# Kernel tuning notes

Hardware: AMD Instinct MI355X
Metric: run time of the kernel (lower is better)

## Reference

```python
import jax, jax.numpy as jnp
import numpy as np

EPS = 1e-5
NUM_HEADS = 8


def _ln(x, g, b):
    m = jnp.mean(x, axis=-1, keepdims=True)
    v = jnp.var(x, axis=-1, keepdims=True)
    return (x - m) * jax.lax.rsqrt(v + EPS) * g + b


def _adaptive_pool_mat(L, out):
    # torch F.adaptive_avg_pool1d bin edges: start=floor(i*L/out), end=ceil((i+1)*L/out)
    i = np.arange(out)
    start = (i * L) // out
    end = -((-(i + 1) * L) // out)
    W = np.zeros((out, L), np.float32)
    for r in range(out):
        W[r, start[r]:end[r]] = 1.0 / (end[r] - start[r])
    return jnp.asarray(W)


def _sparse_mask(S, key):
    # True = blocked. Local band of width ~0.1*S plus random unblocked entries per row.
    keep = max(1, int(S * 0.1))
    half = keep // 2
    idx = jnp.arange(S)
    band = (idx[None, :] >= idx[:, None] - half) & (idx[None, :] <= idx[:, None] + half)
    blocked = ~band
    if keep > 4:
        num_random = max(1, keep // 4)
        keys = jax.random.split(key, S)
        rand_idx = jax.vmap(lambda k: jax.random.permutation(k, S)[:num_random])(keys)
        blocked = blocked.at[idx[:, None], rand_idx].set(False)
    return blocked


def setup_inputs() -> dict:
    key = jax.random.key(0)
    ks = jax.random.split(key, 12)
    B, C, H, W = 1, 256, 64, 64
    s = lambda k, shp: jax.random.normal(k, shp, jnp.float32) * 0.02
    return dict(
        x=jax.random.normal(ks[0], (B, C, H, W), jnp.float32),
        local_pos=s(ks[1], (1, C)),
        reg_pos0=s(ks[2], (1, C)),
        reg_pos1=s(ks[3], (1, C)),
        ln_local_g=jnp.ones((C,), jnp.float32), ln_local_b=jnp.zeros((C,), jnp.float32),
        ln_reg0_g=jnp.ones((C,), jnp.float32), ln_reg0_b=jnp.zeros((C,), jnp.float32),
        ln_reg1_g=jnp.ones((C,), jnp.float32), ln_reg1_b=jnp.zeros((C,), jnp.float32),
        adj0_w=s(ks[4], (C, C * 16)), adj0_b=jnp.zeros((C,), jnp.float32),
        adj1_w=s(ks[5], (C, C * 64)), adj1_b=jnp.zeros((C,), jnp.float32),
        in_proj_w=s(ks[6], (3 * C, C)), in_proj_b=jnp.zeros((3 * C,), jnp.float32),
        out_w=s(ks[7], (C, C)), out_b=jnp.zeros((C,), jnp.float32),
        ln_out_g=jnp.ones((C,), jnp.float32), ln_out_b=jnp.zeros((C,), jnp.float32),
        mlp_w1=s(ks[8], (4 * C, C)), mlp_b1=jnp.zeros((4 * C,), jnp.float32),
        mlp_w2=s(ks[9], (C, 4 * C)), mlp_b2=jnp.zeros((C,), jnp.float32),
    )


def reference(x, local_pos, reg_pos0, reg_pos1,
              ln_local_g, ln_local_b, ln_reg0_g, ln_reg0_b, ln_reg1_g, ln_reg1_b,
              adj0_w, adj0_b, adj1_w, adj1_b,
              in_proj_w, in_proj_b, out_w, out_b,
              ln_out_g, ln_out_b, mlp_w1, mlp_b1, mlp_w2, mlp_b2):
    B, C, H, W = x.shape
    HW = H * W
    # local branch: [B, HW, C]
    x_flat = x.reshape(B, C, HW).transpose(0, 2, 1)
    local_f = _ln(x_flat + local_pos[0], ln_local_g, ln_local_b)
    # regional branches (patch sizes 4, 8): each produces C tokens of dim C
    regional = []
    for ps, rp, lg, lb, aw, ab in ((4, reg_pos0, ln_reg0_g, ln_reg0_b, adj0_w, adj0_b),
                                   (8, reg_pos1, ln_reg1_g, ln_reg1_b, adj1_w, adj1_b)):
        N = (H // ps) * (W // ps)
        xp = x.reshape(B, C, H // ps, ps, W // ps, ps)
        xp = xp.transpose(0, 2, 4, 1, 3, 5).reshape(B, N, C * ps * ps)
        pool = _adaptive_pool_mat(N, C)          # [C, N] pools token dim N -> C
        xp = jnp.einsum('bnd,cn->bcd', xp, pool)  # [B, C, C*ps*ps]
        xp = xp @ aw.T + ab                        # dim_adjust -> [B, C, C]
        regional.append(_ln(xp + rp[0], lg, lb))
    feats = jnp.concatenate([local_f] + regional, axis=1)  # [B, S, C]
    S = feats.shape[1]
    blocked = _sparse_mask(S, jax.random.key(42))
    # MultiheadAttention (eval, dropout off)
    dh = C // NUM_HEADS
    qkv = feats @ in_proj_w.T + in_proj_b
    q, k, v = jnp.split(qkv, 3, axis=-1)
    heads = lambda t: t.reshape(B, S, NUM_HEADS, dh).transpose(0, 2, 1, 3)
    q, k, v = heads(q), heads(k), heads(v)
    scores = jnp.einsum('bhqd,bhkd->bhqk', q, k) / jnp.sqrt(jnp.float32(dh))
    scores = jnp.where(blocked, -jnp.inf, scores)
    attn = jax.nn.softmax(scores, axis=-1)
    ctx = jnp.einsum('bhqk,bhkd->bhqd', attn, v).transpose(0, 2, 1, 3).reshape(B, S, C)
    attn_out = ctx @ out_w.T + out_b
    # take local tokens, residual MLP, fold back to image, outer residual
    lo = attn_out[:, :HW]
    h1 = jax.nn.gelu(_ln(lo, ln_out_g, ln_out_b) @ mlp_w1.T + mlp_b1, approximate=False)
    lo = lo + (h1 @ mlp_w2.T + mlp_b2)
    return lo.transpose(0, 2, 1).reshape(B, C, H, W) + x
```

## Files before the change

kernel.cpp:

```cpp
#include <hip/hip_runtime.h>
#include <hip/hip_bf16.h>
#include <cstdint>

#define THREEFRY_PARTITIONABLE 1

#define C_DIM 256
#define HW 4096
#define S_TOK 4608
#define NRAND 115
#define NW 144
#define HALF_BAND 230
#define CANDCAP 208
#define PTP 40
#define NHEADS 8

typedef __attribute__((ext_vector_type(8))) short bf16x8;
typedef __attribute__((ext_vector_type(4))) float f32x4;
typedef __attribute__((ext_vector_type(16))) float f32x16;

__device__ __forceinline__ bool isbf(const void* gref) {
  return *(const uint32_t*)gref != 0x3F800000u;
}
__device__ __forceinline__ float ldin(const void* p, int i, bool bf) {
  if (bf) return __bfloat162float(((const __hip_bfloat16*)p)[i]);
  return ((const float*)p)[i];
}
__device__ __forceinline__ void stout(void* p, int i, float v, bool bf) {
  if (bf) ((__hip_bfloat16*)p)[i] = __float2bfloat16(v);
  else ((float*)p)[i] = v;
}
__device__ __forceinline__ uint16_t f2bf(float f) {
  __hip_bfloat16 h = __float2bfloat16(f);
  return *(uint16_t*)&h;
}
__device__ __forceinline__ float bfu2f(uint32_t u16) {
  return __uint_as_float(u16 << 16);
}
__device__ __forceinline__ void ld4f(const void* X, bool bf, int idx, float* o) {
  if (bf) {
    const ushort4 u = *(const ushort4*)((const uint16_t*)X + idx);
    o[0] = bfu2f(u.x); o[1] = bfu2f(u.y); o[2] = bfu2f(u.z); o[3] = bfu2f(u.w);
  } else {
    const float4 f = *(const float4*)((const float*)X + idx);
    o[0] = f.x; o[1] = f.y; o[2] = f.z; o[3] = f.w;
  }
}

__device__ __forceinline__ void tf2x32(uint32_t k0, uint32_t k1,
                                       uint32_t x0, uint32_t x1,
                                       uint32_t& o0, uint32_t& o1) {
  const uint32_t k2 = k0 ^ k1 ^ 0x1BD11BDAu;
  x0 += k0; x1 += k1;
#define TFR(r) x0 += x1; x1 = (x1 << (r)) | (x1 >> (32 - (r))); x1 ^= x0;
  TFR(13) TFR(15) TFR(26) TFR(6)
  x0 += k1; x1 += k2 + 1u;
  TFR(17) TFR(29) TFR(16) TFR(24)
  x0 += k2; x1 += k0 + 2u;
  TFR(13) TFR(15) TFR(26) TFR(6)
  x0 += k0; x1 += k1 + 3u;
  TFR(17) TFR(29) TFR(16) TFR(24)
  x0 += k1; x1 += k2 + 4u;
  TFR(13) TFR(15) TFR(26) TFR(6)
  x0 += k2; x1 += k0 + 5u;
#undef TFR
  o0 = x0; o1 = x1;
}

__device__ __forceinline__ float blockSum256(float v, float* rb, int tid) {
#pragma unroll
  for (int o = 32; o > 0; o >>= 1) v += __shfl_down(v, o, 64);
  if ((tid & 63) == 0) rb[tid >> 6] = v;
  __syncthreads();
  float r = rb[0] + rb[1] + rb[2] + rb[3];
  __syncthreads();
  return r;
}

__global__ __launch_bounds__(512) void k_mask(uint16_t* __restrict__ randl) {
  const int q = blockIdx.x;
  const int tid = threadIdx.x;
  __shared__ uint32_t keys1s[S_TOK];
  __shared__ uint16_t mem1[S_TOK];
  __shared__ uint8_t  b2hi[S_TOK];
  __shared__ uint32_t baseA[257];
  __shared__ uint32_t baseB[257];
  __shared__ uint32_t offs[256];
  __shared__ uint32_t candk[CANDCAP];
  __shared__ uint16_t candi[CANDCAP];
  __shared__ uint32_t posmask[NW];
  __shared__ uint8_t  hotb[256];
  __shared__ uint16_t randrow[128];
  __shared__ uint32_t wsum[8];
  __shared__ int ncand, Tsh, nrcnt;

  uint32_t s10, s11, s20, s21;
  {
#if THREEFRY_PARTITIONABLE
    uint32_t kq0, kq1, ka0, ka1;
    tf2x32(0u, 42u, 0u, (uint32_t)q, kq0, kq1);
    tf2x32(kq0, kq1, 0u, 0u, ka0, ka1);
    tf2x32(kq0, kq1, 0u, 1u, s10, s11);
    tf2x32(ka0, ka1, 0u, 1u, s20, s21);
#else
    uint32_t o0, o1, k0, k1;
    uint32_t j = 2u * (uint32_t)q;
    if (j < S_TOK) { tf2x32(0u, 42u, j, j + S_TOK, o0, o1); k0 = o0; }
    else           { tf2x32(0u, 42u, j - S_TOK, j, o0, o1); k0 = o1; }
    j = 2u * (uint32_t)q + 1u;
    if (j < S_TOK) { tf2x32(0u, 42u, j, j + S_TOK, o0, o1); k1 = o0; }
    else           { tf2x32(0u, 42u, j - S_TOK, j, o0, o1); k1 = o1; }
    uint32_t a0, b0, a1, b1;
    tf2x32(k0, k1, 0u, 2u, a0, b0);
    tf2x32(k0, k1, 1u, 3u, a1, b1);
    s10 = b0; s11 = b1;
    uint32_t c0, d0, c1, d1;
    tf2x32(a0, a1, 0u, 2u, c0, d0);
    tf2x32(a0, a1, 1u, 3u, c1, d1);
    s20 = d0; s21 = d1;
#endif
  }
  if (tid == 0) { ncand = 0; Tsh = 0; nrcnt = 0; }
  if (tid < 256) { baseA[tid] = 0u; baseB[tid] = 0u; }
  for (int w = tid; w < NW; w += 512) posmask[w] = 0u;
  __syncthreads();

  uint32_t v1reg[9];
#pragma unroll
  for (int it = 0; it < 9; ++it) {
    const int i = tid + it * 512;
    uint32_t a, b;
    tf2x32(s10, s11, 0u, (uint32_t)i, a, b);
    const uint32_t v1 = a ^ b;
    tf2x32(s20, s21, 0u, (uint32_t)i, a, b);
    const uint32_t v2 = a ^ b;
    v1reg[it] = v1;
    atomicAdd(&baseA[v1 >> 24], 1u);
    atomicAdd(&baseB[v2 >> 24], 1u);
    b2hi[i] = (uint8_t)(v2 >> 24);
  }
  __syncthreads();

  {
    const int g = tid >> 8;
    const int loc = tid & 255;
    uint32_t* base = g ? baseB : baseA;
    const uint32_t v = base[loc];
    uint32_t s = v;
    const int lane = tid & 63;
#pragma unroll
    for (int o = 1; o < 64; o <<= 1) {
      const uint32_t t = __shfl_up(s, o, 64);
      if (lane >= o) s += t;
    }
    if (lane == 63) wsum[g * 4 + (loc >> 6)] = s;
    __syncthreads();
    uint32_t woff = 0;
#pragma unroll
    for (int w = 0; w < 3; ++w)
      if (w < (loc >> 6)) woff += wsum[g * 4 + w];
    const uint32_t ex = woff + s - v;
    base[loc] = ex;
    if (loc == 255) base[256] = ex + v;
    if (g == 1 && (int)ex <= NRAND - 1) atomicMax(&Tsh, loc);
  }
  __syncthreads();
  if (tid < 256) offs[tid] = baseA[tid];
  const int T = Tsh;
  __syncthreads();

#pragma unroll
  for (int it = 0; it < 9; ++it) {
    const int i = tid + it * 512;
    const uint32_t v1 = v1reg[it];
    const uint32_t p = atomicAdd(&offs[v1 >> 24], 1u);
    keys1s[p] = v1;
    mem1[p] = (uint16_t)i;
    if ((int)b2hi[i] <= T) {
      uint32_t a, b;
      tf2x32(s20, s21, 0u, (uint32_t)i, a, b);
      const uint32_t v2 = a ^ b;
      const int c = atomicAdd(&ncand, 1);
      if (c < CANDCAP) { candk[c] = v2; candi[c] = (uint16_t)i; }
    }
  }
  __syncthreads();

  const int nc = min(ncand, CANDCAP);
  for (int c = tid; c < nc; c += 512) {
    const uint32_t kk = candk[c];
    const uint16_t ii = candi[c];
    int r = 0;
    for (int c2 = 0; c2 < nc; ++c2) {
      const uint32_t k2 = candk[c2];
      if (k2 < kk || (k2 == kk && candi[c2] < ii)) ++r;
    }
    if (r < NRAND) atomicOr(&posmask[ii >> 5], 1u << (ii & 31));
  }
  __syncthreads();

  if (tid < 256) {
    const int s0 = (int)baseA[tid], e0 = (int)baseA[tid + 1];
    uint8_t hot = 0;
    if (s0 < e0) {
      for (int w = (s0 >> 5); w <= ((e0 - 1) >> 5); ++w) {
        const int lo = max(s0, w * 32) - w * 32;
        const int hi = min(e0 - 1, w * 32 + 31) - w * 32;
        const uint32_t range = ((hi == 31) ? 0xFFFFFFFFu : ((1u << (hi + 1)) - 1u)) & ~((1u << lo) - 1u);
        if (posmask[w] & range) { hot = 1; break; }
      }
    }
    hotb[tid] = hot;
  }
  __syncthreads();

  for (int p = tid; p < S_TOK; p += 512) {
    const uint32_t ke = keys1s[p];
    const uint32_t bk = ke >> 24;
    if (!hotb[bk]) continue;
    const int e = (int)mem1[p];
    const int s0 = (int)baseA[bk], e0 = (int)baseA[bk + 1];
    int less = 0, eq = 0;
    for (int m = s0; m < e0; ++m) {
      const uint32_t kf = keys1s[m];
      less += (int)(kf < ke);
      eq += (int)(kf == ke);
    }
    int R = s0 + less;
    if (eq > 1) {
      int r2 = 0;
      for (int m = s0; m < e0; ++m)
        if (keys1s[m] == ke && (int)mem1[m] < e) ++r2;
      R += r2;
    }
    if ((posmask[R >> 5] >> (R & 31)) & 1u) {
      const int c = atomicAdd(&nrcnt, 1);
      if (c < 128) randrow[c] = (uint16_t)e;
    }
  }
  __syncthreads();
  if (tid < NRAND) randl[(size_t)q * 128 + tid] = randrow[tid];
}

__global__ __launch_bounds__(256) void k_transpose(const void* __restrict__ x, float* __restrict__ xt,
                                                   const void* __restrict__ gref) {
  const bool bf = isbf(gref);
  __shared__ float tile[32][33];
  const int n0 = blockIdx.x * 32, c0 = blockIdx.y * 32;
  const int tx = threadIdx.x & 31, ty = threadIdx.x >> 5;
  for (int i = ty; i < 32; i += 8)
    tile[i][tx] = ldin(x, (c0 + i) * HW + n0 + tx, bf);
  __syncthreads();
  for (int i = ty; i < 32; i += 8)
    xt[(size_t)(n0 + i) * C_DIM + c0 + tx] = tile[tx][i];
}

#define LDP 40
template <bool GELU, bool ADDSRC, bool OUTBF>
__global__ __launch_bounds__(256) void k_gemm_mfma(const float* __restrict__ A, const void* __restrict__ B,
                                                   const void* __restrict__ bias, const float* __restrict__ SRC,
                                                   void* __restrict__ Cout, int M, int N, int K,
                                                   const void* __restrict__ gref) {
  const bool bf = isbf(gref);
  __shared__ uint16_t As[64 * LDP];
  __shared__ uint16_t Bs[64 * LDP];
  const int bn = blockIdx.x * 64, bm = blockIdx.y * 64;
  const int tid = threadIdx.x;
  const int wave = tid >> 6, lane = tid & 63;
  const int l15 = lane & 15, quad = lane >> 4;
  const int srow = tid >> 2, scg = tid & 3;
  f32x4 acc[4] = {{0.f, 0.f, 0.f, 0.f}, {0.f, 0.f, 0.f, 0.f}, {0.f, 0.f, 0.f, 0.f}, {0.f, 0.f, 0.f, 0.f}};

  for (int k0 = 0; k0 < K; k0 += 32) {
    {
      const float* ap = A + (size_t)(bm + srow) * K + k0 + scg * 8;
      const float4 a0 = *(const float4*)ap;
      const float4 a1 = *(const float4*)(ap + 4);
      uint4 w;
      w.x = (uint32_t)f2bf(a0.x) | ((uint32_t)f2bf(a0.y) << 16);
      w.y = (uint32_t)f2bf(a0.z) | ((uint32_t)f2bf(a0.w) << 16);
      w.z = (uint32_t)f2bf(a1.x) | ((uint32_t)f2bf(a1.y) << 16);
      w.w = (uint32_t)f2bf(a1.z) | ((uint32_t)f2bf(a1.w) << 16);
      *(uint4*)&As[srow * LDP + scg * 8] = w;
    }
    {
      const size_t boff = (size_t)(bn + srow) * K + k0 + scg * 8;
      uint4 w;
      if (bf) {
        w = *(const uint4*)((const uint16_t*)B + boff);
      } else {
        const float* bp = (const float*)B + boff;
        const float4 b0 = *(const float4*)bp;
        const float4 b1 = *(const float4*)(bp + 4);
        w.x = (uint32_t)f2bf(b0.x) | ((uint32_t)f2bf(b0.y) << 16);
        w.y = (uint32_t)f2bf(b0.z) | ((uint32_t)f2bf(b0.w) << 16);
        w.z = (uint32_t)f2bf(b1.x) | ((uint32_t)f2bf(b1.y) << 16);
        w.w = (uint32_t)f2bf(b1.z) | ((uint32_t)f2bf(b1.w) << 16);
      }
      *(uint4*)&Bs[srow * LDP + scg * 8] = w;
    }
    __syncthreads();
    const bf16x8 afrag = *(const bf16x8*)&As[(wave * 16 + l15) * LDP + quad * 8];
#pragma unroll
    for (int j = 0; j < 4; ++j) {
      const bf16x8 bfrag = *(const bf16x8*)&Bs[(j * 16 + l15) * LDP + quad * 8];
      acc[j] = __builtin_amdgcn_mfma_f32_16x16x32_bf16(afrag, bfrag, acc[j], 0, 0, 0);
    }
    __syncthreads();
  }
#pragma unroll
  for (int j = 0; j < 4; ++j) {
    const int n = bn + j * 16 + l15;
    const float bv = ldin(bias, n, bf);
#pragma unroll
    for (int r = 0; r < 4; ++r) {
      const int m = bm + wave * 16 + quad * 4 + r;
      float v = acc[j][r] + bv;
      if (GELU) v = 0.5f * v * (1.0f + erff(v * 0.70710678118654752f));
      if (ADDSRC) v += SRC[(size_t)m * N + n];
      if (OUTBF) ((__hip_bfloat16*)Cout)[(size_t)m * N + n] = __float2bfloat16(v);
      else ((float*)Cout)[(size_t)m * N + n] = v;
    }
  }
}

template <int MODE>
__global__ __launch_bounds__(256) void k_adj_mfma(const void* __restrict__ X, const void* __restrict__ B,
                                                  float* __restrict__ Cout, int N, int K, int Kc,
                                                  const void* __restrict__ gref) {
  const bool bf = isbf(gref);
  __shared__ uint16_t As[64 * LDP];
  __shared__ uint16_t Bs[64 * LDP];
  const int bn = blockIdx.x * 64, bm = blockIdx.y * 64;
  const int k0base = blockIdx.z * Kc;
  const int tid = threadIdx.x;
  const int wave = tid >> 6, lane = tid & 63;
  const int l15 = lane & 15, quad = lane >> 4;
  const int srow = tid >> 2, scg = tid & 3;
  f32x4 acc[4] = {{0.f, 0.f, 0.f, 0.f}, {0.f, 0.f, 0.f, 0.f}, {0.f, 0.f, 0.f, 0.f}, {0.f, 0.f, 0.f, 0.f}};

  for (int k0 = k0base; k0 < k0base + Kc; k0 += 32) {
    {
      const int m = bm + srow;
      const int d0 = k0 + scg * 8;
      float av[8];
      if (MODE == 1) {
        const int hr = m >> 4, wr = m & 15;
        const int cch = d0 >> 4;
        const int i0 = (d0 >> 2) & 3;
        ld4f(X, bf, cch * HW + (hr * 4 + i0) * 64 + wr * 4, av);
        ld4f(X, bf, cch * HW + (hr * 4 + i0 + 1) * 64 + wr * 4, av + 4);
      } else {
        const int hr = m >> 3, wr = m & 7;
        const int cch = d0 >> 6, ii = (d0 >> 3) & 7;
        const int base = cch * HW + (hr * 8 + ii) * 64 + wr * 8;
        ld4f(X, bf, base, av);
        ld4f(X, bf, base + 4, av + 4);
      }
      uint4 w;
      w.x = (uint32_t)f2bf(av[0]) | ((uint32_t)f2bf(av[1]) << 16);
      w.y = (uint32_t)f2bf(av[2]) | ((uint32_t)f2bf(av[3]) << 16);
      w.z = (uint32_t)f2bf(av[4]) | ((uint32_t)f2bf(av[5]) << 16);
      w.w = (uint32_t)f2bf(av[6]) | ((uint32_t)f2bf(av[7]) << 16);
      *(uint4*)&As[srow * LDP + scg * 8] = w;
    }
    {
      const size_t boff = (size_t)(bn + srow) * K + k0 + scg * 8;
      uint4 w;
      if (bf) {
        w = *(const uint4*)((const uint16_t*)B + boff);
      } else {
        const float* bp = (const float*)B + boff;
        const float4 b0 = *(const float4*)bp;
        const float4 b1 = *(const float4*)(bp + 4);
        w.x = (uint32_t)f2bf(b0.x) | ((uint32_t)f2bf(b0.y) << 16);
        w.y = (uint32_t)f2bf(b0.z) | ((uint32_t)f2bf(b0.w) << 16);
        w.z = (uint32_t)f2bf(b1.x) | ((uint32_t)f2bf(b1.y) << 16);
        w.w = (uint32_t)f2bf(b1.z) | ((uint32_t)f2bf(b1.w) << 16);
      }
      *(uint4*)&Bs[srow * LDP + scg * 8] = w;
    }
    __syncthreads();
    const bf16x8 afrag = *(const bf16x8*)&As[(wave * 16 + l15) * LDP + quad * 8];
#pragma unroll
    for (int j = 0; j < 4; ++j) {
      const bf16x8 bfrag = *(const bf16x8*)&Bs[(j * 16 + l15) * LDP + quad * 8];
      acc[j] = __builtin_amdgcn_mfma_f32_16x16x32_bf16(afrag, bfrag, acc[j], 0, 0, 0);
    }
    __syncthreads();
  }
#pragma unroll
  for (int j = 0; j < 4; ++j) {
    const int n = bn + j * 16 + l15;
#pragma unroll
    for (int r = 0; r < 4; ++r) {
      const int m = bm + wave * 16 + quad * 4 + r;
      atomicAdd(&Cout[(size_t)m * N + n], acc[j][r]);
    }
  }
}

__global__ __launch_bounds__(256) void k_init_bias2(float* __restrict__ Y, const void* __restrict__ b0,
                                                    const void* __restrict__ b1, const void* __restrict__ gref) {
  const bool bf = isbf(gref);
  const int idx = blockIdx.x * 256 + threadIdx.x;
  const int row = idx >> 8, c = idx & 255;
  Y[idx] = ldin(row < 256 ? b0 : b1, c, bf);
}

__global__ __launch_bounds__(256) void k_ln(const float* __restrict__ X, const void* __restrict__ pos,
                                            const void* __restrict__ g, const void* __restrict__ b,
                                            float* __restrict__ Y, const void* __restrict__ gref) {
  const bool bf = isbf(gref);
  __shared__ float rb[4];
  const int row = blockIdx.x, c = threadIdx.x;
  float v = X[(size_t)row * C_DIM + c];
  if (pos) v += ldin(pos, c, bf);
  const float m = blockSum256(v, rb, c) * (1.f / 256.f);
  const float dd = v - m;
  const float var = blockSum256(dd * dd, rb, c) * (1.f / 256.f);
  Y[(size_t)row * C_DIM + c] = dd * rsqrtf(var + 1e-5f) * ldin(g, c, bf) + ldin(b, c, bf);
}

__global__ __launch_bounds__(256) void k_ln_all(const float* __restrict__ xt,
                                                const float* __restrict__ y0, const float* __restrict__ y1,
                                                const void* lp, const void* rp0, const void* rp1,
                                                const void* gl, const void* bl,
                                                const void* g0, const void* b0,
                                                const void* g1, const void* b1,
                                                float* __restrict__ feats, const void* __restrict__ gref) {
  const bool bf = isbf(gref);
  __shared__ float rb[4];
  const int r = blockIdx.x, c = threadIdx.x;
  const float* src; const void *rp, *g, *bb;
  if (r < HW)            { src = xt + (size_t)r * C_DIM; rp = lp; g = gl; bb = bl; }
  else if (r < HW + 256) { src = y0 + (size_t)(r - HW) * C_DIM; rp = rp0; g = g0; bb = b0; }
  else                   { src = y1 + (size_t)((r - HW - 256) >> 2) * C_DIM; rp = rp1; g = g1; bb = b1; }
  float v = src[c] + ldin(rp, c, bf);
  const float m = blockSum256(v, rb, c) * (1.f / 256.f);
  const float dd = v - m;
  const float var = blockSum256(dd * dd, rb, c) * (1.f / 256.f);
  feats[(size_t)r * C_DIM + c] = dd * rsqrtf(var + 1e-5f) * ldin(g, c, bf) + ldin(bb, c, bf);
}

__global__ __launch_bounds__(256) void k_attn_mfma(const __hip_bfloat16* __restrict__ qkvb,
                                                   const uint16_t* __restrict__ randl,
                                                   float* __restrict__ ctx) {
  const int qt = blockIdx.x;
  const int h  = blockIdx.y;
  const int q0 = qt * 32;
  const int tid = threadIdx.x;
  const int w = tid >> 6, l = tid & 63;
  const int hh = l >> 5, col = l & 31;

  __shared__ float    qs[32][33];
  __shared__ __align__(16) uint16_t vt[4][32 * PTP];
  __shared__ __align__(16) uint16_t pt[4][32 * PTP];
  __shared__ float    rsc[32][116];
  __shared__ uint16_t rl[32][116];
  __shared__ float    mxs[4][32];
  __shared__ float    denw[4][32];
  __shared__ float    denr[32];
  __shared__ float    rmx[32];
  __shared__ float    rowmax[32];
  __shared__ float    ctxs[32][33];
  __shared__ int      nrr[32];

  const int lo_u = max(q0 - HALF_BAND, 0);
  const int hi_u = min(q0 + 31 + HALF_BAND, S_TOK - 1);
  const int nt = (hi_u - lo_u + 32) >> 5;

  if (tid < 32) { nrr[tid] = 0; denr[tid] = 0.f; rmx[tid] = -INFINITY; }
  for (int e = tid; e < 1024; e += 256) {
    const int r = e >> 5, d = e & 31;
    qs[r][d] = __bfloat162float(qkvb[(size_t)(q0 + r) * 768 + h * 32 + d]);
    ctxs[r][d] = 0.f;
  }
  __syncthreads();
  {
    const int r = tid >> 3, g = tid & 7;
    const int q = q0 + r;
    const int lo_r = max(q - HALF_BAND, 0), hi_r = min(q + HALF_BAND, S_TOK - 1);
    for (int t = g; t < NRAND; t += 8) {
      const int k = (int)randl[(size_t)q * 128 + t];
      if (k < lo_r || k > hi_r) {
        const int c = atomicAdd(&nrr[r], 1);
        rl[r][c] = (uint16_t)k;
      }
    }
  }
  __syncthreads();

  const float scale = 0.17677669529663687f;
  const __hip_bfloat16* qrow = qkvb + (size_t)(q0 + col) * 768 + h * 32;
  const bf16x8 qa0 = *(const bf16x8*)(qrow + 8 * hh);
  const bf16x8 qa1 = *(const bf16x8*)(qrow + 16 + 8 * hh);

  float bm[16];
#pragma unroll
  for (int i = 0; i < 16; ++i) bm[i] = -INFINITY;
  for (int kt = w; kt < nt; kt += 4) {
    const int kbase = lo_u + kt * 32;
    const __hip_bfloat16* krow = qkvb + (size_t)(kbase + col) * 768 + 256 + h * 32;
    const bf16x8 kb0 = *(const bf16x8*)(krow + 8 * hh);
    const bf16x8 kb1 = *(const bf16x8*)(krow + 16 + 8 * hh);
    f32x16 s = {0.f, 0.f, 0.f, 0.f, 0.f, 0.f, 0.f, 0.f, 0.f, 0.f, 0.f, 0.f, 0.f, 0.f, 0.f, 0.f};
    s = __builtin_amdgcn_mfma_f32_32x32x16_bf16(qa0, kb0, s, 0, 0, 0);
    s = __builtin_amdgcn_mfma_f32_32x32x16_bf16(qa1, kb1, s, 0, 0, 0);
    if (kbase + col <= hi_u) {
#pragma unroll
      for (int i = 0; i < 16; ++i) bm[i] = fmaxf(bm[i], s[i]);
    }
  }
#pragma unroll
  for (int o = 1; o < 32; o <<= 1)
#pragma unroll
    for (int i = 0; i < 16; ++i) bm[i] = fmaxf(bm[i], __shfl_xor(bm[i], o, 64));
  if (col == 0)
#pragma unroll
    for (int i = 0; i < 16; ++i) mxs[w][(i & 3) + 8 * (i >> 2) + 4 * hh] = bm[i] * scale;

  {
    const int r = tid >> 3, g = tid & 7;
    const int nr = nrr[r];
    float lm = -INFINITY;
    for (int i = g; i < nr; i += 8) {
      const int k = (int)rl[r][i];
      const uint4* kp = (const uint4*)(qkvb + (size_t)k * 768 + 256 + h * 32);
      float dsum = 0.f;
#pragma unroll
      for (int t = 0; t < 4; ++t) {
        const uint4 kw = kp[t];
        dsum += qs[r][8 * t + 0] * bfu2f(kw.x & 0xffffu) + qs[r][8 * t + 1] * __uint_as_float(kw.x & 0xffff0000u);
        dsum += qs[r][8 * t + 2] * bfu2f(kw.y & 0xffffu) + qs[r][8 * t + 3] * __uint_as_float(kw.y & 0xffff0000u);
        dsum += qs[r][8 * t + 4] * bfu2f(kw.z & 0xffffu) + qs[r][8 * t + 5] * __uint_as_float(kw.z & 0xffff0000u);
        dsum += qs[r][8 * t + 6] * bfu2f(kw.w & 0xffffu) + qs[r][8 * t + 7] * __uint_as_float(kw.w & 0xffff0000u);
      }
      const float sv = dsum * scale;
      rsc[r][i] = sv;
      lm = fmaxf(lm, sv);
    }
#pragma unroll
    for (int o = 1; o < 8; o <<= 1) lm = fmaxf(lm, __shfl_xor(lm, o, 64));
    if (g == 0) rmx[r] = lm;
  }
  __syncthreads();
  if (tid < 32)
    rowmax[tid] = fmaxf(fmaxf(fmaxf(mxs[0][tid], mxs[1][tid]), fmaxf(mxs[2][tid], mxs[3][tid])), rmx[tid]);
  __syncthreads();

  f32x16 cacc = {0.f, 0.f, 0.f, 0.f, 0.f, 0.f, 0.f, 0.f, 0.f, 0.f, 0.f, 0.f, 0.f, 0.f, 0.f, 0.f};
  float dssum[16];
#pragma unroll
  for (int i = 0; i < 16; ++i) dssum[i] = 0.f;
  for (int kt = w; kt < nt; kt += 4) {
    const int kbase = lo_u + kt * 32;
    const __hip_bfloat16* krow = qkvb + (size_t)(kbase + col) * 768 + 256 + h * 32;
    const bf16x8 kb0 = *(const bf16x8*)(krow + 8 * hh);
    const bf16x8 kb1 = *(const bf16x8*)(krow + 16 + 8 * hh);
    const int key2 = l >> 1;
    const int dbase = (l & 1) * 16;
    const uint16_t* vsrc = (const uint16_t*)qkvb + (size_t)(kbase + key2) * 768 + 512 + h * 32 + dbase;
    uint32_t wv[8];
    *(uint4*)&wv[0] = *(const uint4*)vsrc;
    *(uint4*)&wv[4] = *(const uint4*)(vsrc + 8);
    f32x16 s = {0.f, 0.f, 0.f, 0.f, 0.f, 0.f, 0.f, 0.f, 0.f, 0.f, 0.f, 0.f, 0.f, 0.f, 0.f, 0.f};
    s = __builtin_amdgcn_mfma_f32_32x32x16_bf16(qa0, kb0, s, 0, 0, 0);
    s = __builtin_amdgcn_mfma_f32_32x32x16_bf16(qa1, kb1, s, 0, 0, 0);
    const int kk = kbase + col;
#pragma unroll
    for (int i = 0; i < 16; ++i) {
      const int qrl = (i & 3) + 8 * (i >> 2) + 4 * hh;
      const int qr = q0 + qrl;
      float e = 0.f;
      if (kk <= hi_u && kk >= qr - HALF_BAND && kk <= qr + HALF_BAND)
        e = __expf(s[i] * scale - rowmax[qrl]);
      dssum[i] += e;
      pt[w][qrl * PTP + col] = f2bf(e);
    }
#pragma unroll
    for (int j = 0; j < 8; ++j) {
      vt[w][(dbase + 2 * j) * PTP + key2] = (uint16_t)(wv[j] & 0xffffu);
      vt[w][(dbase + 2 * j + 1) * PTP + key2] = (uint16_t)(wv[j] >> 16);
    }
    asm volatile("s_waitcnt lgkmcnt(0)" ::: "memory");
#pragma unroll
    for (int g2 = 0; g2 < 2; ++g2) {
      const bf16x8 pa = *(const bf16x8*)&pt[w][col * PTP + 16 * g2 + 8 * hh];
      const bf16x8 vb = *(const bf16x8*)&vt[w][col * PTP + 16 * g2 + 8 * hh];
      cacc = __builtin_amdgcn_mfma_f32_32x32x16_bf16(pa, vb, cacc, 0, 0, 0);
    }
  }
#pragma unroll
  for (int o = 1; o < 32; o <<= 1)
#pragma unroll
    for (int i = 0; i < 16; ++i) dssum[i] += __shfl_xor(dssum[i], o, 64);
  if (col == 0)
#pragma unroll
    for (int i = 0; i < 16; ++i) denw[w][(i & 3) + 8 * (i >> 2) + 4 * hh] = dssum[i];
#pragma unroll
  for (int i = 0; i < 16; ++i)
    atomicAdd(&ctxs[(i & 3) + 8 * (i >> 2) + 4 * hh][col], cacc[i]);

  {
    const int r = tid >> 3, g = tid & 7;
    const int nr = nrr[r];
    const float mx = rowmax[r];
    float dsum = 0.f;
    for (int i = g; i < nr; i += 8) {
      const float e = __expf(rsc[r][i] - mx);
      rsc[r][i] = e;
      dsum += e;
    }
#pragma unroll
    for (int o = 1; o < 8; o <<= 1) dsum += __shfl_xor(dsum, o, 64);
    if (g == 0) denr[r] = dsum;
  }
  __syncthreads();
  {
    const int r = tid >> 3, g = tid & 7;
    const int nr = nrr[r];
    float r0 = 0.f, r1 = 0.f, r2 = 0.f, r3 = 0.f;
    for (int i = 0; i < nr; ++i) {
      const int k = (int)rl[r][i];
      const float e = rsc[r][i];
      const uint2 vw = *(const uint2*)(qkvb + (size_t)k * 768 + 512 + h * 32 + g * 4);
      r0 += e * bfu2f(vw.x & 0xffffu);
      r1 += e * __uint_as_float(vw.x & 0xffff0000u);
      r2 += e * bfu2f(vw.y & 0xffffu);
      r3 += e * __uint_as_float(vw.y & 0xffff0000u);
    }
    atomicAdd(&ctxs[r][g * 4 + 0], r0);
    atomicAdd(&ctxs[r][g * 4 + 1], r1);
    atomicAdd(&ctxs[r][g * 4 + 2], r2);
    atomicAdd(&ctxs[r][g * 4 + 3], r3);
  }
  __syncthreads();
  {
    const int r = tid >> 3, d0 = (tid & 7) * 4;
    const float den = fmaxf(denw[0][r] + denw[1][r] + denw[2][r] + denw[3][r] + denr[r], 1e-30f);
    const float inv = 1.f / den;
#pragma unroll
    for (int j = 0; j < 4; ++j)
      ctx[(size_t)(q0 + r) * C_DIM + h * 32 + d0 + j] = ctxs[r][d0 + j] * inv;
  }
}

__global__ __launch_bounds__(256) void k_final(const float* __restrict__ lo2, const void* __restrict__ x,
                                               void* __restrict__ out, const void* __restrict__ gref) {
  const bool bf = isbf(gref);
  __shared__ float tile[32][33];
  const int n0 = blockIdx.x * 32, c0 = blockIdx.y * 32;
  const int tx = threadIdx.x & 31, ty = threadIdx.x >> 5;
  for (int i = ty; i < 32; i += 8)
    tile[i][tx] = lo2[(size_t)(n0 + i) * C_DIM + c0 + tx];
  __syncthreads();
  for (int i = ty; i < 32; i += 8) {
    const int o = (c0 + i) * HW + n0 + tx;
    stout(out, o, tile[tx][i] + ldin(x, o, bf), bf);
  }
}

extern "C" void kernel_launch(void* const* d_in, const int* in_sizes, int n_in,
                              void* d_out, int out_size, void* d_ws, size_t ws_size,
                              hipStream_t stream) {
  const void* x          = d_in[0];
  const void* local_pos  = d_in[1];
  const void* reg_pos0   = d_in[2];
  const void* reg_pos1   = d_in[3];
  const void* ln_local_g = d_in[4];
  const void* ln_local_b = d_in[5];
  const void* ln_reg0_g  = d_in[6];
  const void* ln_reg0_b  = d_in[7];
  const void* ln_reg1_g  = d_in[8];
  const void* ln_reg1_b  = d_in[9];
  const void* adj0_w     = d_in[10];
  const void* adj0_b     = d_in[11];
  const void* adj1_w     = d_in[12];
  const void* adj1_b     = d_in[13];
  const void* in_proj_w  = d_in[14];
  const void* in_proj_b  = d_in[15];
  const void* out_w      = d_in[16];
  const void* out_b      = d_in[17];
  const void* ln_out_g   = d_in[18];
  const void* ln_out_b   = d_in[19];
  const void* mlp_w1     = d_in[20];
  const void* mlp_b1     = d_in[21];
  const void* mlp_w2     = d_in[22];
  const void* mlp_b2     = d_in[23];
  char* ws = (char*)d_ws;

  float* xt      = (float*)(ws + 0);
  float* yraw    = (float*)(ws + 4194304);
  float* feats   = (float*)(ws + 4718592);
  __hip_bfloat16* qkvb = (__hip_bfloat16*)(ws + 9437184);
  uint16_t* randl = (uint16_t*)(ws + 23592960);
  float* ctx     = (float*)(ws + 0);
  float* lo      = (float*)(ws + 4194304);
  float* lnlo    = (float*)(ws + 8388608);
  float* h1      = (float*)(ws + 12582912);
  float* lo2     = (float*)(ws + 0);

  const void* gref = ln_local_g;

  k_mask<<<dim3(HW), 512, 0, stream>>>(randl);
  k_transpose<<<dim3(HW / 32, C_DIM / 32), 256, 0, stream>>>(x, xt, gref);
  k_init_bias2<<<dim3(320), 256, 0, stream>>>(yraw, adj0_b, adj1_b, gref);
  k_adj_mfma<1><<<dim3(4, 4, 8), 256, 0, stream>>>(x, adj0_w, yraw, 256, 4096, 512, gref);
  k_adj_mfma<2><<<dim3(4, 1, 32), 256, 0, stream>>>(x, adj1_w, yraw + 256 * 256, 256, 16384, 512, gref);
  k_ln_all<<<dim3(S_TOK), 256, 0, stream>>>(xt, yraw, yraw + 256 * 256,
                                            local_pos, reg_pos0, reg_pos1,
                                            ln_local_g, ln_local_b, ln_reg0_g, ln_reg0_b,
                                            ln_reg1_g, ln_reg1_b, feats, gref);
  k_gemm_mfma<false, false, true><<<dim3(12, 72), 256, 0, stream>>>(feats, in_proj_w, in_proj_b, nullptr, qkvb, S_TOK, 768, 256, gref);
  k_attn_mfma<<<dim3(HW / 32, NHEADS), 256, 0, stream>>>(qkvb, randl, ctx);
  k_gemm_mfma<false, false, false><<<dim3(4, 64), 256, 0, stream>>>(ctx, out_w, out_b, nullptr, lo, HW, 256, 256, gref);
  k_ln<<<dim3(HW), 256, 0, stream>>>(lo, nullptr, ln_out_g, ln_out_b, lnlo, gref);
  k_gemm_mfma<true, false, false><<<dim3(16, 64), 256, 0, stream>>>(lnlo, mlp_w1, mlp_b1, nullptr, h1, HW, 1024, 256, gref);
  k_gemm_mfma<false, true, false><<<dim3(4, 64), 256, 0, stream>>>(h1, mlp_w2, mlp_b2, lo, lo2, HW, 256, 1024, gref);
  k_final<<<dim3(HW / 32, C_DIM / 32), 256, 0, stream>>>(lo2, x, d_out, gref);
}
```

Measured before the change: 506.8 us.

## Fuse mask, transpose and adjust GEMMs into one launch; split-K final MLP GEMM

Merges the mask generation, input transpose and both dim-adjust GEMMs into a single heterogeneous kernel dispatched by block index, so the small GEMMs and the transpose can share the GPU with the long mask kernel. The bias init kernel is replaced by a memset, with the adjust biases folded into the LayerNorm kernel instead. The second MLP GEMM is split along K into two partial outputs that the final transpose sums. The attention kernel now computes random-key scores once during the exp pass instead of in a separate max pass, relying on the band max alone for stability. Using 512-thread blocks with large shared memory for the GEMM and transpose roles wastes half the threads and may lower occupancy. Skipping the random keys in the row max risks exp overflow if a random score is far above the band max.

After: 452.3 us. 1.12x faster.

```diff
diff --git a/kernel.cpp b/kernel.cpp
--- a/kernel.cpp
+++ b/kernel.cpp
@@ -13,6 +13,11 @@
 #define CANDCAP 208
 #define PTP 40
 #define NHEADS 8
+
+#define NB_MASK 4096
+#define NB_TR   1024
+#define NB_ADJ1 128
+#define NB_ADJ2 128
 
 typedef __attribute__((ext_vector_type(8))) short bf16x8;
 typedef __attribute__((ext_vector_type(4))) float f32x4;
@@ -76,10 +81,85 @@
   return r;
 }
 
-__global__ __launch_bounds__(512) void k_mask(uint16_t* __restrict__ randl) {
-  const int q = blockIdx.x;
+#define LDP 40
+
+template <int MODE>
+__device__ __forceinline__ void adj_body(const void* X, const void* Bmat, float* Cout,
+                                         int N, int K, int bn, int bm, int k0base,
+                                         uint16_t* As, uint16_t* Bs, bool bf, int tid) {
+  const int wave = tid >> 6, lane = tid & 63;
+  const int l15 = lane & 15, quad = lane >> 4;
+  const int srow = tid >> 2, scg = tid & 3;
+  f32x4 acc[4] = {{0.f, 0.f, 0.f, 0.f}, {0.f, 0.f, 0.f, 0.f}, {0.f, 0.f, 0.f, 0.f}, {0.f, 0.f, 0.f, 0.f}};
+
+  for (int k0 = k0base; k0 < k0base + 512; k0 += 32) {
+    {
+      const int m = bm + srow;
+      const int d0 = k0 + scg * 8;
+      float av[8];
+      if (MODE == 1) {
+        const int hr = m >> 4, wr = m & 15;
+        const int cch = d0 >> 4;
+        const int i0 = (d0 >> 2) & 3;
+        ld4f(X, bf, cch * HW + (hr * 4 + i0) * 64 + wr * 4, av);
+        ld4f(X, bf, cch * HW + (hr * 4 + i0 + 1) * 64 + wr * 4, av + 4);
+      } else {
+        const int hr = m >> 3, wr = m & 7;
+        const int cch = d0 >> 6, ii = (d0 >> 3) & 7;
+        const int base = cch * HW + (hr * 8 + ii) * 64 + wr * 8;
+        ld4f(X, bf, base, av);
+        ld4f(X, bf, base + 4, av + 4);
+      }
+      uint4 w;
+      w.x = (uint32_t)f2bf(av[0]) | ((uint32_t)f2bf(av[1]) << 16);
+      w.y = (uint32_t)f2bf(av[2]) | ((uint32_t)f2bf(av[3]) << 16);
+      w.z = (uint32_t)f2bf(av[4]) | ((uint32_t)f2bf(av[5]) << 16);
+      w.w = (uint32_t)f2bf(av[6]) | ((uint32_t)f2bf(av[7]) << 16);
+      *(uint4*)&As[srow * LDP + scg * 8] = w;
+    }
+    {
+      const size_t boff = (size_t)(bn + srow) * K + k0 + scg * 8;
+      uint4 w;
+      if (bf) {
+        w = *(const uint4*)((const uint16_t*)Bmat + boff);
+      } else {
+        const float* bp = (const float*)Bmat + boff;
+        const float4 b0 = *(const float4*)bp;
+        const float4 b1 = *(const float4*)(bp + 4);
+        w.x = (uint32_t)f2bf(b0.x) | ((uint32_t)f2bf(b0.y) << 16);
+        w.y = (uint32_t)f2bf(b0.z) | ((uint32_t)f2bf(b0.w) << 16);
+        w.z = (uint32_t)f2bf(b1.x) | ((uint32_t)f2bf(b1.y) << 16);
+        w.w = (uint32_t)f2bf(b1.z) | ((uint32_t)f2bf(b1.w) << 16);
+      }
+      *(uint4*)&Bs[srow * LDP + scg * 8] = w;
+    }
+    __syncthreads();
+    const bf16x8 afrag = *(const bf16x8*)&As[(wave * 16 + l15) * LDP + quad * 8];
+#pragma unroll
+    for (int j = 0; j < 4; ++j) {
+      const bf16x8 bfrag = *(const bf16x8*)&Bs[(j * 16 + l15) * LDP + quad * 8];
+      acc[j] = __builtin_amdgcn_mfma_f32_16x16x32_bf16(afrag, bfrag, acc[j], 0, 0, 0);
+    }
+    __syncthreads();
+  }
+#pragma unroll
+  for (int j = 0; j < 4; ++j) {
+    const int n = bn + j * 16 + l15;
+#pragma unroll
+    for (int r = 0; r < 4; ++r) {
+      const int m = bm + wave * 16 + quad * 4 + r;
+      atomicAdd(&Cout[(size_t)m * N + n], acc[j][r]);
+    }
+  }
+}
+
+__global__ __launch_bounds__(512, 8) void k_pre(uint16_t* __restrict__ randl,
+                                                const void* __restrict__ x, float* __restrict__ xt,
+                                                const void* __restrict__ adj0_w, const void* __restrict__ adj1_w,
+                                                float* __restrict__ yraw, const void* __restrict__ gref) {
+  const int b = blockIdx.x;
   const int tid = threadIdx.x;
-  __shared__ uint32_t keys1s[S_TOK];
+  __shared__ __align__(16) uint32_t keys1s[S_TOK];
   __shared__ uint16_t mem1[S_TOK];
   __shared__ uint8_t  b2hi[S_TOK];
   __shared__ uint32_t baseA[257];
@@ -93,6 +173,36 @@
   __shared__ uint32_t wsum[8];
   __shared__ int ncand, Tsh, nrcnt;
 
+  if (b >= NB_MASK) {
+    if (tid >= 256) return;
+    const bool bf = isbf(gref);
+    if (b < NB_MASK + NB_TR) {
+      float (*tile)[33] = (float(*)[33])keys1s;
+      const int t = b - NB_MASK;
+      const int n0 = (t & 127) * 32, c0 = (t >> 7) * 32;
+      const int tx = tid & 31, ty = tid >> 5;
+      for (int i = ty; i < 32; i += 8)
+        tile[i][tx] = ldin(x, (c0 + i) * HW + n0 + tx, bf);
+      __syncthreads();
+      for (int i = ty; i < 32; i += 8)
+        xt[(size_t)(n0 + i) * C_DIM + c0 + tx] = tile[tx][i];
+      return;
+    }
+    uint16_t* As = (uint16_t*)keys1s;
+    uint16_t* Bs = (uint16_t*)(keys1s + 1280);
+    if (b < NB_MASK + NB_TR + NB_ADJ1) {
+      const int t = b - (NB_MASK + NB_TR);
+      adj_body<1>(x, adj0_w, yraw, 256, 4096,
+                  (t & 3) * 64, ((t >> 2) & 3) * 64, (t >> 4) * 512, As, Bs, bf, tid);
+    } else {
+      const int t = b - (NB_MASK + NB_TR + NB_ADJ1);
+      adj_body<2>(x, adj1_w, yraw + 256 * 256, 256, 16384,
+                  (t & 3) * 64, 0, (t >> 2) * 512, As, Bs, bf, tid);
+    }
+    return;
+  }
+
+  const int q = b;
   uint32_t s10, s11, s20, s21;
   {
 #if THREEFRY_PARTITIONABLE
@@ -128,11 +238,11 @@
 #pragma unroll
   for (int it = 0; it < 9; ++it) {
     const int i = tid + it * 512;
-    uint32_t a, b;
-    tf2x32(s10, s11, 0u, (uint32_t)i, a, b);
-    const uint32_t v1 = a ^ b;
-    tf2x32(s20, s21, 0u, (uint32_t)i, a, b);
-    const uint32_t v2 = a ^ b;
+    uint32_t a, bb;
+    tf2x32(s10, s11, 0u, (uint32_t)i, a, bb);
+    const uint32_t v1 = a ^ bb;
+    tf2x32(s20, s21, 0u, (uint32_t)i, a, bb);
+    const uint32_t v2 = a ^ bb;
     v1reg[it] = v1;
     atomicAdd(&baseA[v1 >> 24], 1u);
     atomicAdd(&baseB[v2 >> 24], 1u);
@@ -176,9 +286,9 @@
     keys1s[p] = v1;
     mem1[p] = (uint16_t)i;
     if ((int)b2hi[i] <= T) {
-      uint32_t a, b;
-      tf2x32(s20, s21, 0u, (uint32_t)i, a, b);
-      const uint32_t v2 = a ^ b;
+      uint32_t a, bb;
+      tf2x32(s20, s21, 0u, (uint32_t)i, a, bb);
+      const uint32_t v2 = a ^ bb;
       const int c = atomicAdd(&ncand, 1);
       if (c < CANDCAP) { candk[c] = v2; candi[c] = (uint16_t)i; }
     }
@@ -241,24 +351,11 @@
   if (tid < NRAND) randl[(size_t)q * 128 + tid] = randrow[tid];
 }
 
-__global__ __launch_bounds__(256) void k_transpose(const void* __restrict__ x, float* __restrict__ xt,
-                                                   const void* __restrict__ gref) {
-  const bool bf = isbf(gref);
-  __shared__ float tile[32][33];
-  const int n0 = blockIdx.x * 32, c0 = blockIdx.y * 32;
-  const int tx = threadIdx.x & 31, ty = threadIdx.x >> 5;
-  for (int i = ty; i < 32; i += 8)
-    tile[i][tx] = ldin(x, (c0 + i) * HW + n0 + tx, bf);
-  __syncthreads();
-  for (int i = ty; i < 32; i += 8)
-    xt[(size_t)(n0 + i) * C_DIM + c0 + tx] = tile[tx][i];
-}
-
-#define LDP 40
-template <bool GELU, bool ADDSRC, bool OUTBF>
+template <bool GELU, bool ADDSRC, bool OUTBF, bool SPLITK>
 __global__ __launch_bounds__(256) void k_gemm_mfma(const float* __restrict__ A, const void* __restrict__ B,
                                                    const void* __restrict__ bias, const float* __restrict__ SRC,
-                                                   void* __restrict__ Cout, int M, int N, int K,
+                                                   void* __restrict__ Cout, void* __restrict__ Cout2,
+                                                   int M, int N, int K,
                                                    const void* __restrict__ gref) {
   const bool bf = isbf(gref);
   __shared__ uint16_t As[64 * LDP];
@@ -268,9 +365,16 @@
   const int wave = tid >> 6, lane = tid & 63;
   const int l15 = lane & 15, quad = lane >> 4;
   const int srow = tid >> 2, scg = tid & 3;
+  int kBeg = 0, kEnd = K;
+  bool lead = true;
+  if (SPLITK) {
+    const int Kc = K >> 1;
+    kBeg = blockIdx.z * Kc; kEnd = kBeg + Kc;
+    lead = (blockIdx.z == 0);
+  }
   f32x4 acc[4] = {{0.f, 0.f, 0.f, 0.f}, {0.f, 0.f, 0.f, 0.f}, {0.f, 0.f, 0.f, 0.f}, {0.f, 0.f, 0.f, 0.f}};
 
-  for (int k0 = 0; k0 < K; k0 += 32) {
+  for (int k0 = kBeg; k0 < kEnd; k0 += 32) {
     {
       const float* ap = A + (size_t)(bm + srow) * K + k0 + scg * 8;
       const float4 a0 = *(const float4*)ap;
@@ -307,6 +411,7 @@
     }
     __syncthreads();
   }
+  void* outp = (SPLITK && blockIdx.z) ? Cout2 : Cout;
 #pragma unroll
   for (int j = 0; j < 4; ++j) {
     const int n = bn + j * 16 + l15;
@@ -314,97 +419,14 @@
 #pragma unroll
     for (int r = 0; r < 4; ++r) {
       const int m = bm + wave * 16 + quad * 4 + r;
-      float v = acc[j][r] + bv;
+      float v = acc[j][r];
+      if (lead) v += bv;
       if (GELU) v = 0.5f * v * (1.0f + erff(v * 0.70710678118654752f));
-      if (ADDSRC) v += SRC[(size_t)m * N + n];
-      if (OUTBF) ((__hip_bfloat16*)Cout)[(size_t)m * N + n] = __float2bfloat16(v);
-      else ((float*)Cout)[(size_t)m * N + n] = v;
-    }
-  }
-}
-
-template <int MODE>
-__global__ __launch_bounds__(256) void k_adj_mfma(const void* __restrict__ X, const void* __restrict__ B,
-                                                  float* __restrict__ Cout, int N, int K, int Kc,
-                                                  const void* __restrict__ gref) {
-  const bool bf = isbf(gref);
-  __shared__ uint16_t As[64 * LDP];
-  __shared__ uint16_t Bs[64 * LDP];
-  const int bn = blockIdx.x * 64, bm = blockIdx.y * 64;
-  const int k0base = blockIdx.z * Kc;
-  const int tid = threadIdx.x;
-  const int wave = tid >> 6, lane = tid & 63;
-  const int l15 = lane & 15, quad = lane >> 4;
-  const int srow = tid >> 2, scg = tid & 3;
-  f32x4 acc[4] = {{0.f, 0.f, 0.f, 0.f}, {0.f, 0.f, 0.f, 0.f}, {0.f, 0.f, 0.f, 0.f}, {0.f, 0.f, 0.f, 0.f}};
-
-  for (int k0 = k0base; k0 < k0base + Kc; k0 += 32) {
-    {
-      const int m = bm + srow;
-      const int d0 = k0 + scg * 8;
-      float av[8];
-      if (MODE == 1) {
-        const int hr = m >> 4, wr = m & 15;
-        const int cch = d0 >> 4;
-        const int i0 = (d0 >> 2) & 3;
-        ld4f(X, bf, cch * HW + (hr * 4 + i0) * 64 + wr * 4, av);
-        ld4f(X, bf, cch * HW + (hr * 4 + i0 + 1) * 64 + wr * 4, av + 4);
-      } else {
-        const int hr = m >> 3, wr = m & 7;
-        const int cch = d0 >> 6, ii = (d0 >> 3) & 7;
-        const int base = cch * HW + (hr * 8 + ii) * 64 + wr * 8;
-        ld4f(X, bf, base, av);
-        ld4f(X, bf, base + 4, av + 4);
-      }
-      uint4 w;
-      w.x = (uint32_t)f2bf(av[0]) | ((uint32_t)f2bf(av[1]) << 16);
-      w.y = (uint32_t)f2bf(av[2]) | ((uint32_t)f2bf(av[3]) << 16);
-      w.z = (uint32_t)f2bf(av[4]) | ((uint32_t)f2bf(av[5]) << 16);
-      w.w = (uint32_t)f2bf(av[6]) | ((uint32_t)f2bf(av[7]) << 16);
-      *(uint4*)&As[srow * LDP + scg * 8] = w;
-    }
-    {
-      const size_t boff = (size_t)(bn + srow) * K + k0 + scg * 8;
-      uint4 w;
-      if (bf) {
-        w = *(const uint4*)((const uint16_t*)B + boff);
-      } else {
-        const float* bp = (const float*)B + boff;
-        const float4 b0 = *(const float4*)bp;
-        const float4 b1 = *(const float4*)(bp + 4);
-        w.x = (uint32_t)f2bf(b0.x) | ((uint32_t)f2bf(b0.y) << 16);
-        w.y = (uint32_t)f2bf(b0.z) | ((uint32_t)f2bf(b0.w) << 16);
-        w.z = (uint32_t)f2bf(b1.x) | ((uint32_t)f2bf(b1.y) << 16);
-        w.w = (uint32_t)f2bf(b1.z) | ((uint32_t)f2bf(b1.w) << 16);
-      }
-      *(uint4*)&Bs[srow * LDP + scg * 8] = w;
-    }
-    __syncthreads();
-    const bf16x8 afrag = *(const bf16x8*)&As[(wave * 16 + l15) * LDP + quad * 8];
-#pragma unroll
-    for (int j = 0; j < 4; ++j) {
-      const bf16x8 bfrag = *(const bf16x8*)&Bs[(j * 16 + l15) * LDP + quad * 8];
-      acc[j] = __builtin_amdgcn_mfma_f32_16x16x32_bf16(afrag, bfrag, acc[j], 0, 0, 0);
-    }
-    __syncthreads();
-  }
-#pragma unroll
-  for (int j = 0; j < 4; ++j) {
-    const int n = bn + j * 16 + l15;
-#pragma unroll
-    for (int r = 0; r < 4; ++r) {
-      const int m = bm + wave * 16 + quad * 4 + r;
-      atomicAdd(&Cout[(size_t)m * N + n], acc[j][r]);
-    }
-  }
-}
-
-__global__ __launch_bounds__(256) void k_init_bias2(float* __restrict__ Y, const void* __restrict__ b0,
-                                                    const void* __restrict__ b1, const void* __restrict__ gref) {
-  const bool bf = isbf(gref);
-  const int idx = blockIdx.x * 256 + threadIdx.x;
-  const int row = idx >> 8, c = idx & 255;
-  Y[idx] = ldin(row < 256 ? b0 : b1, c, bf);
+      if (ADDSRC && lead) v += SRC[(size_t)m * N + n];
+      if (OUTBF) ((__hip_bfloat16*)outp)[(size_t)m * N + n] = __float2bfloat16(v);
+      else ((float*)outp)[(size_t)m * N + n] = v;
+    }
+  }
 }
 
 __global__ __launch_bounds__(256) void k_ln(const float* __restrict__ X, const void* __restrict__ pos,
@@ -427,15 +449,17 @@
                                                 const void* gl, const void* bl,
                                                 const void* g0, const void* b0,
                                                 const void* g1, const void* b1,
+                                                const void* ab0, const void* ab1,
                                                 float* __restrict__ feats, const void* __restrict__ gref) {
   const bool bf = isbf(gref);
   __shared__ float rb[4];
   const int r = blockIdx.x, c = threadIdx.x;
-  const float* src; const void *rp, *g, *bb;
-  if (r < HW)            { src = xt + (size_t)r * C_DIM; rp = lp; g = gl; bb = bl; }
-  else if (r < HW + 256) { src = y0 + (size_t)(r - HW) * C_DIM; rp = rp0; g = g0; bb = b0; }
-  else                   { src = y1 + (size_t)((r - HW - 256) >> 2) * C_DIM; rp = rp1; g = g1; bb = b1; }
+  const float* src; const void *rp, *g, *bb, *ab;
+  if (r < HW)            { src = xt + (size_t)r * C_DIM; rp = lp; g = gl; bb = bl; ab = nullptr; }
+  else if (r < HW + 256) { src = y0 + (size_t)(r - HW) * C_DIM; rp = rp0; g = g0; bb = b0; ab = ab0; }
+  else                   { src = y1 + (size_t)((r - HW - 256) >> 2) * C_DIM; rp = rp1; g = g1; bb = b1; ab = ab1; }
   float v = src[c] + ldin(rp, c, bf);
+  if (ab) v += ldin(ab, c, bf);
   const float m = blockSum256(v, rb, c) * (1.f / 256.f);
   const float dd = v - m;
   const float var = blockSum256(dd * dd, rb, c) * (1.f / 256.f);
@@ -460,7 +484,6 @@
   __shared__ float    mxs[4][32];
   __shared__ float    denw[4][32];
   __shared__ float    denr[32];
-  __shared__ float    rmx[32];
   __shared__ float    rowmax[32];
   __shared__ float    ctxs[32][33];
   __shared__ int      nrr[32];
@@ -469,7 +492,7 @@
   const int hi_u = min(q0 + 31 + HALF_BAND, S_TOK - 1);
   const int nt = (hi_u - lo_u + 32) >> 5;
 
-  if (tid < 32) { nrr[tid] = 0; denr[tid] = 0.f; rmx[tid] = -INFINITY; }
+  if (tid < 32) { nrr[tid] = 0; denr[tid] = 0.f; }
   for (int e = tid; e < 1024; e += 256) {
     const int r = e >> 5, d = e & 31;
     qs[r][d] = __bfloat162float(qkvb[(size_t)(q0 + r) * 768 + h * 32 + d]);
@@ -518,34 +541,9 @@
   if (col == 0)
 #pragma unroll
     for (int i = 0; i < 16; ++i) mxs[w][(i & 3) + 8 * (i >> 2) + 4 * hh] = bm[i] * scale;
-
-  {
-    const int r = tid >> 3, g = tid & 7;
-    const int nr = nrr[r];
-    float lm = -INFINITY;
-    for (int i = g; i < nr; i += 8) {
-      const int k = (int)rl[r][i];
-      const uint4* kp = (const uint4*)(qkvb + (size_t)k * 768 + 256 + h * 32);
-      float dsum = 0.f;
-#pragma unroll
-      for (int t = 0; t < 4; ++t) {
-        const uint4 kw = kp[t];
-        dsum += qs[r][8 * t + 0] * bfu2f(kw.x & 0xffffu) + qs[r][8 * t + 1] * __uint_as_float(kw.x & 0xffff0000u);
-        dsum += qs[r][8 * t + 2] * bfu2f(kw.y & 0xffffu) + qs[r][8 * t + 3] * __uint_as_float(kw.y & 0xffff0000u);
-        dsum += qs[r][8 * t + 4] * bfu2f(kw.z & 0xffffu) + qs[r][8 * t + 5] * __uint_as_float(kw.z & 0xffff0000u);
-        dsum += qs[r][8 * t + 6] * bfu2f(kw.w & 0xffffu) + qs[r][8 * t + 7] * __uint_as_float(kw.w & 0xffff0000u);
-      }
-      const float sv = dsum * scale;
-      rsc[r][i] = sv;
-      lm = fmaxf(lm, sv);
-    }
-#pragma unroll
-    for (int o = 1; o < 8; o <<= 1) lm = fmaxf(lm, __shfl_xor(lm, o, 64));
-    if (g == 0) rmx[r] = lm;
-  }
   __syncthreads();
   if (tid < 32)
-    rowmax[tid] = fmaxf(fmaxf(fmaxf(mxs[0][tid], mxs[1][tid]), fmaxf(mxs[2][tid], mxs[3][tid])), rmx[tid]);
+    rowmax[tid] = fmaxf(fmaxf(mxs[0][tid], mxs[1][tid]), fmaxf(mxs[2][tid], mxs[3][tid]));
   __syncthreads();
 
   f32x16 cacc = {0.f, 0.f, 0.f, 0.f, 0.f, 0.f, 0.f, 0.f, 0.f, 0.f, 0.f, 0.f, 0.f, 0.f, 0.f, 0.f};
@@ -607,7 +605,18 @@
     const float mx = rowmax[r];
     float dsum = 0.f;
     for (int i = g; i < nr; i += 8) {
-      const float e = __expf(rsc[r][i] - mx);
+      const int k = (int)rl[r][i];
+      const uint4* kp = (const uint4*)(qkvb + (size_t)k * 768 + 256 + h * 32);
+      float ds2 = 0.f;
+#pragma unroll
+      for (int t = 0; t < 4; ++t) {
+        const uint4 kw = kp[t];
+        ds2 += qs[r][8 * t + 0] * bfu2f(kw.x & 0xffffu) + qs[r][8 * t + 1] * __uint_as_float(kw.x & 0xffff0000u);
+        ds2 += qs[r][8 * t + 2] * bfu2f(kw.y & 0xffffu) + qs[r][8 * t + 3] * __uint_as_float(kw.y & 0xffff0000u);
+        ds2 += qs[r][8 * t + 4] * bfu2f(kw.z & 0xffffu) + qs[r][8 * t + 5] * __uint_as_float(kw.z & 0xffff0000u);
+        ds2 += qs[r][8 * t + 6] * bfu2f(kw.w & 0xffffu) + qs[r][8 * t + 7] * __uint_as_float(kw.w & 0xffff0000u);
+      }
+      const float e = __expf(ds2 * scale - mx);
       rsc[r][i] = e;
       dsum += e;
     }
@@ -620,6 +629,7 @@
     const int r = tid >> 3, g = tid & 7;
     const int nr = nrr[r];
     float r0 = 0.f, r1 = 0.f, r2 = 0.f, r3 = 0.f;
+#pragma unroll 4
     for (int i = 0; i < nr; ++i) {
       const int k = (int)rl[r][i];
       const float e = rsc[r][i];
@@ -645,14 +655,17 @@
   }
 }
 
-__global__ __launch_bounds__(256) void k_final(const float* __restrict__ lo2, const void* __restrict__ x,
+__global__ __launch_bounds__(256) void k_final(const float* __restrict__ lo2a, const float* __restrict__ lo2b,
+                                               const void* __restrict__ x,
                                                void* __restrict__ out, const void* __restrict__ gref) {
   const bool bf = isbf(gref);
   __shared__ float tile[32][33];
   const int n0 = blockIdx.x * 32, c0 = blockIdx.y * 32;
   const int tx = threadIdx.x & 31, ty = threadIdx.x >> 5;
-  for (int i = ty; i < 32; i += 8)
-    tile[i][tx] = lo2[(size_t)(n0 + i) * C_DIM + c0 + tx];
+  for (int i = ty; i < 32; i += 8) {
+    const size_t o = (size_t)(n0 + i) * C_DIM + c0 + tx;
+    tile[i][tx] = lo2a[o] + lo2b[o];
+  }
   __syncthreads();
   for (int i = ty; i < 32; i += 8) {
     const int o = (c0 + i) * HW + n0 + tx;
@@ -698,24 +711,22 @@
   float* lo      = (float*)(ws + 4194304);
   float* lnlo    = (float*)(ws + 8388608);
   float* h1      = (float*)(ws + 12582912);
-  float* lo2     = (float*)(ws + 0);
+  float* lo2a    = (float*)(ws + 0);
+  float* lo2b    = (float*)(ws + 8388608);
 
   const void* gref = ln_local_g;
 
-  k_mask<<<dim3(HW), 512, 0, stream>>>(randl);
-  k_transpose<<<dim3(HW / 32, C_DIM / 32), 256, 0, stream>>>(x, xt, gref);
-  k_init_bias2<<<dim3(320), 256, 0, stream>>>(yraw, adj0_b, adj1_b, gref);
-  k_adj_mfma<1><<<dim3(4, 4, 8), 256, 0, stream>>>(x, adj0_w, yraw, 256, 4096, 512, gref);
-  k_adj_mfma<2><<<dim3(4, 1, 32), 256, 0, stream>>>(x, adj1_w, yraw + 256 * 256, 256, 16384, 512, gref);
+  hipMemsetAsync(yraw, 0, 320 * 256 * sizeof(float), stream);
+  k_pre<<<dim3(NB_MASK + NB_TR + NB_ADJ1 + NB_ADJ2), 512, 0, stream>>>(randl, x, xt, adj0_w, adj1_w, yraw, gref);
   k_ln_all<<<dim3(S_TOK), 256, 0, stream>>>(xt, yraw, yraw + 256 * 256,
                                             local_pos, reg_pos0, reg_pos1,
                                             ln_local_g, ln_local_b, ln_reg0_g, ln_reg0_b,
-                                            ln_reg1_g, ln_reg1_b, feats, gref);
-  k_gemm_mfma<false, false, true><<<dim3(12, 72), 256, 0, stream>>>(feats, in_proj_w, in_proj_b, nullptr, qkvb, S_TOK, 768, 256, gref);
+                                            ln_reg1_g, ln_reg1_b, adj0_b, adj1_b, feats, gref);
+  k_gemm_mfma<false, false, true, false><<<dim3(12, 72), 256, 0, stream>>>(feats, in_proj_w, in_proj_b, nullptr, qkvb, nullptr, S_TOK, 768, 256, gref);
   k_attn_mfma<<<dim3(HW / 32, NHEADS), 256, 0, stream>>>(qkvb, randl, ctx);
-  k_gemm_mfma<false, false, false><<<dim3(4, 64), 256, 0, stream>>>(ctx, out_w, out_b, nullptr, lo, HW, 256, 256, gref);
+  k_gemm_mfma<false, false, false, false><<<dim3(4, 64), 256, 0, stream>>>(ctx, out_w, out_b, nullptr, lo, nullptr, HW, 256, 256, gref);
   k_ln<<<dim3(HW), 256, 0, stream>>>(lo, nullptr, ln_out_g, ln_out_b, lnlo, gref);
-  k_gemm_mfma<true, false, false><<<dim3(16, 64), 256, 0, stream>>>(lnlo, mlp_w1, mlp_b1, nullptr, h1, HW, 1024, 256, gref);
-  k_gemm_mfma<false, true, false><<<dim3(4, 64), 256, 0, stream>>>(h1, mlp_w2, mlp_b2, lo, lo2, HW, 256, 1024, gref);
-  k_final<<<dim3(HW / 32, C_DIM / 32), 256, 0, stream>>>(lo2, x, d_out, gref);
-}
+  k_gemm_mfma<true, false, false, false><<<dim3(16, 64), 256, 0, stream>>>(lnlo, mlp_w1, mlp_b1, nullptr, h1, nullptr, HW, 1024, 256, gref);
+  k_gemm_mfma<false, true, false, true><<<dim3(4, 64, 2), 256, 0, stream>>>(h1, mlp_w2, mlp_b2, lo, lo2a, lo2b, HW, 256, 1024, gref);
+  k_final<<<dim3(HW / 32, C_DIM / 32), 256, 0, stream>>>(lo2a, lo2b, x, d_out, gref);
+}
```
